# Optimization experiments

Measured on AMD Instinct MI355X. Metric: run time of the kernel, lower is better.

The kernel has to match this reference:

```python
import jax, jax.numpy as jnp
import numpy as np

T, B, I_DIM, H_DIM = 256, 64, 1024, 1024


def setup_inputs() -> dict:
    key = jax.random.key(0)
    k_in, k_wx, k_wh = jax.random.split(key, 3)
    # xavier-normal-ish scale for [hidden, input] matrices
    std_x = float(np.sqrt(2.0 / (I_DIM + H_DIM)))
    std_h = float(np.sqrt(2.0 / (H_DIM + H_DIM)))
    return {
        "inputs": jax.random.normal(k_in, (T, B, I_DIM), dtype=jnp.float32),
        "W_x": jax.random.normal(k_wx, (4, H_DIM, I_DIM), dtype=jnp.float32) * std_x,
        "W_h": jax.random.normal(k_wh, (4, H_DIM, H_DIM), dtype=jnp.float32) * std_h,
        "bias": jnp.zeros((4, H_DIM), dtype=jnp.float32),
        "mask_x": jnp.ones((4, H_DIM, I_DIM), dtype=jnp.float32),
        "mask_h": jnp.ones((4, H_DIM, H_DIM), dtype=jnp.float32),
        "H0": jnp.zeros((B, H_DIM), dtype=jnp.float32),
        "C0": jnp.zeros((B, H_DIM), dtype=jnp.float32),
    }


def reference(inputs, W_x, W_h, bias, mask_x, mask_h, H0, C0):
    # masked + transposed weights: (4, in_dim, hidden) so X @ W works
    Wx_t = jnp.transpose(W_x * mask_x, (0, 2, 1))  # (4, I, H)
    Wh_t = jnp.transpose(W_h * mask_h, (0, 2, 1))  # (4, H, H)

    # gate order per original indexing: 0=i, 1=f, 2=o, 3=c
    def step(carry, X):
        H, C = carry
        # fused gate GEMMs: (4, B, H)
        g = (jnp.einsum('bi,gih->gbh', X, Wx_t)
             + jnp.einsum('bh,ghk->gbk', H, Wh_t)
             + bias[:, None, :])
        I_g = jax.nn.sigmoid(g[0])
        F_g = jax.nn.sigmoid(g[1])
        O_g = jax.nn.sigmoid(g[2])
        C_t = jnp.tanh(g[3])
        C_new = F_g * C + I_g * C_t
        H_new = O_g * jnp.tanh(C_new)
        return (H_new, C_new), H_new

    (_, _), outputs = jax.lax.scan(step, (H0, C0), inputs)
    return outputs  # (T, B, H)
```

## Files before the change

kernel.cpp:

```cpp
#include <hip/hip_runtime.h>

typedef __attribute__((ext_vector_type(8))) short short8;
typedef __attribute__((ext_vector_type(4))) float floatx4;

#define T_STEPS 256
#define BATCH   64
#define IDIM    1024
#define HDIM    1024
#define KDIM    (IDIM + HDIM)
#define MB      16
#define HB      16
#define NWG     256
#define NTHR    512
#define A_STRIDE (KDIM + 8)

__device__ __forceinline__ unsigned short f2bf(float f) {
  unsigned u = __float_as_uint(f);
  u += 0x7FFFu + ((u >> 16) & 1u);
  return (unsigned short)(u >> 16);
}

__global__ void prep_weights(const float* __restrict__ Wx, const float* __restrict__ Wh,
                             const float* __restrict__ mx, const float* __restrict__ mh,
                             unsigned short* __restrict__ Wcat) {
  int idx = blockIdx.x * blockDim.x + threadIdx.x;
  const int total = 4 * HDIM * KDIM / 4;
  if (idx >= total) return;
  int k4 = idx & (KDIM / 4 - 1);
  int gh = idx >> 9;
  int k = k4 * 4;
  float4 v, m;
  if (k < IDIM) {
    v = *(const float4*)(Wx + (size_t)gh * IDIM + k);
    m = *(const float4*)(mx + (size_t)gh * IDIM + k);
  } else {
    v = *(const float4*)(Wh + (size_t)gh * HDIM + (k - IDIM));
    m = *(const float4*)(mh + (size_t)gh * HDIM + (k - IDIM));
  }
  ushort4 o;
  o.x = f2bf(v.x * m.x); o.y = f2bf(v.y * m.y);
  o.z = f2bf(v.z * m.z); o.w = f2bf(v.w * m.w);
  *(ushort4*)(Wcat + (size_t)gh * KDIM + k) = o;
}

__global__ void prep_h0(const float* __restrict__ H0, unsigned short* __restrict__ Hbuf0,
                        unsigned* __restrict__ cnt) {
  int i = blockIdx.x * blockDim.x + threadIdx.x;
  if (i < BATCH * HDIM) Hbuf0[i] = f2bf(H0[i]);
  if (i < 16 * 16) cnt[i] = 0u;
}

__global__ void __launch_bounds__(NTHR, 2)
lstm_main(const float* __restrict__ X,
          const float* __restrict__ bias,
          const float* __restrict__ C0,
          const unsigned short* __restrict__ Wcat,
          unsigned short* __restrict__ Hbuf0,
          unsigned short* __restrict__ Hbuf1,
          unsigned* __restrict__ cnt,
          float* __restrict__ out)
{
  __shared__ __align__(16) unsigned short Ash[MB * A_STRIDE];
  __shared__ float parts[2][4][MB][HB + 1];

  const int tid  = threadIdx.x;
  const int wg   = blockIdx.x;
  const int bg   = wg >> 6;
  const int hg   = wg & 63;
  const int b0   = bg * MB;
  const int h0   = hg * HB;

  const int w    = tid >> 6;
  const int lane = tid & 63;
  const int nl   = lane & 15;
  const int quad = lane >> 4;

  short8 Bfr[4][8];
  {
    const short8* wp = (const short8*)Wcat;
#pragma unroll
    for (int g = 0; g < 4; ++g) {
      const int rowbase = (g * HDIM + h0 + nl) * (KDIM / 8);
#pragma unroll
      for (int ks = 0; ks < 8; ++ks)
        Bfr[g][ks] = wp[rowbase + w * 32 + ks * 4 + quad];
    }
  }

  float c_state = 0.f;
  const int eb = tid >> 4;
  const int eh = tid & 15;
  if (tid < 256) c_state = C0[(b0 + eb) * HDIM + h0 + eh];

  const int e0 = tid, e1 = tid + NTHR;
  const int p0 = (e0 >> 8) * (MB * (HB + 1)) + ((e0 >> 4) & 15) * (HB + 1) + (e0 & 15);
  const int p1 = (e1 >> 8) * (MB * (HB + 1)) + ((e1 >> 4) & 15) * (HB + 1) + (e1 & 15);
  const float binit0 = bias[(e0 >> 8) * HDIM + h0 + (e0 & 15)];
  const float binit1 = bias[(e1 >> 8) * HDIM + h0 + (e1 & 15)];

  const int c8 = tid & 127;
  const int mrow = tid >> 7;

  unsigned* mycnt  = cnt + (bg * 4 + (hg & 3)) * 16;
  unsigned* bgcnt  = cnt + bg * 4 * 16;

  float4 Xpre[8];
  {
    const float4* xp = (const float4*)(X + (size_t)b0 * IDIM);
#pragma unroll
    for (int it = 0; it < 8; ++it) {
      int v = it * NTHR + tid;
      Xpre[it] = xp[(v >> 8) * (IDIM / 4) + (v & 255)];
    }
  }

  for (int t = 0; t < T_STEPS; ++t) {
    const unsigned short* __restrict__ Hprev = (t & 1) ? Hbuf1 : Hbuf0;
    unsigned short* __restrict__ Hnext       = (t & 1) ? Hbuf0 : Hbuf1;
    float* pcur = &parts[t & 1][0][0][0];

#pragma unroll
    for (int it = 0; it < 8; ++it) {
      int v = it * NTHR + tid;
      int m = v >> 8, c4 = v & 255;
      float4 f = Xpre[it];
      ushort4 o;
      o.x = f2bf(f.x); o.y = f2bf(f.y); o.z = f2bf(f.z); o.w = f2bf(f.w);
      *(ushort4*)&Ash[m * A_STRIDE + c4 * 4] = o;
    }
    pcur[p0] = binit0;
    pcur[p1] = binit1;

    if (tid == 0 && t > 0) {
      const unsigned tgt = (unsigned)(64 * t);
      for (;;) {
        unsigned s = __hip_atomic_load(bgcnt +  0, __ATOMIC_RELAXED, __HIP_MEMORY_SCOPE_AGENT)
                   + __hip_atomic_load(bgcnt + 16, __ATOMIC_RELAXED, __HIP_MEMORY_SCOPE_AGENT)
                   + __hip_atomic_load(bgcnt + 32, __ATOMIC_RELAXED, __HIP_MEMORY_SCOPE_AGENT)
                   + __hip_atomic_load(bgcnt + 48, __ATOMIC_RELAXED, __HIP_MEMORY_SCOPE_AGENT);
        if (s >= tgt) break;
        __builtin_amdgcn_s_sleep(8);
      }
    }
    __syncthreads();

    {
      const unsigned short* pa = Hprev + (size_t)(b0 + mrow) * HDIM + c8 * 8;
      uint4 d0, d1, d2, d3;
      asm volatile(
        "global_load_dwordx4 %0, %4, off sc0 sc1\n\t"
        "global_load_dwordx4 %1, %5, off sc0 sc1\n\t"
        "global_load_dwordx4 %2, %6, off sc0 sc1\n\t"
        "global_load_dwordx4 %3, %7, off sc0 sc1\n\t"
        "s_waitcnt vmcnt(0)"
        : "=&v"(d0), "=&v"(d1), "=&v"(d2), "=&v"(d3)
        : "v"(pa), "v"(pa + 4 * HDIM), "v"(pa + 8 * HDIM), "v"(pa + 12 * HDIM)
        : "memory");
      *(uint4*)&Ash[(mrow +  0) * A_STRIDE + IDIM + c8 * 8] = d0;
      *(uint4*)&Ash[(mrow +  4) * A_STRIDE + IDIM + c8 * 8] = d1;
      *(uint4*)&Ash[(mrow +  8) * A_STRIDE + IDIM + c8 * 8] = d2;
      *(uint4*)&Ash[(mrow + 12) * A_STRIDE + IDIM + c8 * 8] = d3;
    }
    __syncthreads();

    {
      int tn = (t + 1 < T_STEPS) ? t + 1 : t;
      const float4* xp = (const float4*)(X + ((size_t)tn * BATCH + b0) * IDIM);
#pragma unroll
      for (int it = 0; it < 8; ++it) {
        int v = it * NTHR + tid;
        Xpre[it] = xp[(v >> 8) * (IDIM / 4) + (v & 255)];
      }
    }

    floatx4 acc[4];
#pragma unroll
    for (int g = 0; g < 4; ++g) acc[g] = floatx4{0.f, 0.f, 0.f, 0.f};
    {
      const unsigned short* abase = &Ash[nl * A_STRIDE + w * 256 + quad * 8];
#pragma unroll
      for (int ks = 0; ks < 8; ++ks) {
        short8 af = *(const short8*)(abase + ks * 32);
#pragma unroll
        for (int g = 0; g < 4; ++g)
          acc[g] = __builtin_amdgcn_mfma_f32_16x16x32_bf16(af, Bfr[g][ks], acc[g], 0, 0, 0);
      }
    }
#pragma unroll
    for (int g = 0; g < 4; ++g)
#pragma unroll
      for (int r = 0; r < 4; ++r)
        atomicAdd(&parts[t & 1][g][quad * 4 + r][nl], acc[g][r]);
    __syncthreads();

    if (tid < 256) {
      float gI = parts[t & 1][0][eb][eh];
      float gF = parts[t & 1][1][eb][eh];
      float gO = parts[t & 1][2][eb][eh];
      float gC = parts[t & 1][3][eb][eh];
      float ig = 1.f / (1.f + __expf(-gI));
      float fg = 1.f / (1.f + __expf(-gF));
      float og = 1.f / (1.f + __expf(-gO));
      float cb = 1.f - 2.f / (__expf(2.f * gC) + 1.f);
      c_state = fg * c_state + ig * cb;
      float hn = og * (1.f - 2.f / (__expf(2.f * c_state) + 1.f));
      unsigned short hb = f2bf(hn);
      unsigned short* ps = Hnext + (size_t)(b0 + eb) * HDIM + h0 + eh;
      asm volatile("global_store_short %0, %1, off sc0 sc1"
                   :: "v"(ps), "v"((unsigned)hb) : "memory");
      out[((size_t)t * BATCH + b0 + eb) * HDIM + h0 + eh] = hn;
    }
    asm volatile("s_waitcnt vmcnt(0)" ::: "memory");
    __syncthreads();
    if (tid == 0) atomicAdd(mycnt, 1u);
  }
}

extern "C" void kernel_launch(void* const* d_in, const int* in_sizes, int n_in,
                              void* d_out, int out_size, void* d_ws, size_t ws_size,
                              hipStream_t stream) {
  const float* X    = (const float*)d_in[0];
  const float* Wx   = (const float*)d_in[1];
  const float* Wh   = (const float*)d_in[2];
  const float* bias = (const float*)d_in[3];
  const float* mx   = (const float*)d_in[4];
  const float* mh   = (const float*)d_in[5];
  const float* H0   = (const float*)d_in[6];
  const float* C0   = (const float*)d_in[7];
  float* out = (float*)d_out;

  unsigned short* Wcat  = (unsigned short*)d_ws;
  unsigned short* Hbuf0 = Wcat + (size_t)4 * HDIM * KDIM;
  unsigned short* Hbuf1 = Hbuf0 + BATCH * HDIM;
  unsigned*       cnt   = (unsigned*)(Hbuf1 + BATCH * HDIM);

  {
    int tot = 4 * HDIM * KDIM / 4;
    prep_weights<<<(tot + 255) / 256, 256, 0, stream>>>(Wx, Wh, mx, mh, Wcat);
  }
  prep_h0<<<(BATCH * HDIM + 255) / 256, 256, 0, stream>>>(H0, Hbuf0, cnt);

  void* args[] = { (void*)&X, (void*)&bias, (void*)&C0, (void*)&Wcat,
                   (void*)&Hbuf0, (void*)&Hbuf1, (void*)&cnt, (void*)&out };
  hipLaunchCooperativeKernel(reinterpret_cast<void*>(lstm_main),
                             dim3(NWG), dim3(NTHR), args, 0, stream);
}
```

Baseline: 3.477 ms.

## Split waves into X-input and H-recurrent roles, drop LDS staging and block barriers

```diff
diff --git a/kernel.cpp b/kernel.cpp
--- a/kernel.cpp
+++ b/kernel.cpp
@@ -12,7 +12,7 @@
 #define HB      16
 #define NWG     256
 #define NTHR    512
-#define A_STRIDE (KDIM + 8)
+#define NSUB    8
 
 __device__ __forceinline__ unsigned short f2bf(float f) {
   unsigned u = __float_as_uint(f);
@@ -47,7 +47,7 @@
                         unsigned* __restrict__ cnt) {
   int i = blockIdx.x * blockDim.x + threadIdx.x;
   if (i < BATCH * HDIM) Hbuf0[i] = f2bf(H0[i]);
-  if (i < 16 * 16) cnt[i] = 0u;
+  if (i < 4 * NSUB * 16) cnt[i] = 0u;
 }
 
 __global__ void __launch_bounds__(NTHR, 2)
@@ -60,7 +60,6 @@
           unsigned* __restrict__ cnt,
           float* __restrict__ out)
 {
-  __shared__ __align__(16) unsigned short Ash[MB * A_STRIDE];
   __shared__ float parts[2][4][MB][HB + 1];
 
   const int tid  = threadIdx.x;
@@ -87,105 +86,97 @@
     }
   }
 
+  for (int i = tid; i < 2 * 4 * MB * (HB + 1); i += NTHR)
+    (&parts[0][0][0][0])[i] = 0.f;
+
   float c_state = 0.f;
   const int eb = tid >> 4;
   const int eh = tid & 15;
   if (tid < 256) c_state = C0[(b0 + eb) * HDIM + h0 + eh];
 
-  const int e0 = tid, e1 = tid + NTHR;
-  const int p0 = (e0 >> 8) * (MB * (HB + 1)) + ((e0 >> 4) & 15) * (HB + 1) + (e0 & 15);
-  const int p1 = (e1 >> 8) * (MB * (HB + 1)) + ((e1 >> 4) & 15) * (HB + 1) + (e1 & 15);
-  const float binit0 = bias[(e0 >> 8) * HDIM + h0 + (e0 & 15)];
-  const float binit1 = bias[(e1 >> 8) * HDIM + h0 + (e1 & 15)];
-
-  const int c8 = tid & 127;
-  const int mrow = tid >> 7;
-
-  unsigned* mycnt  = cnt + (bg * 4 + (hg & 3)) * 16;
-  unsigned* bgcnt  = cnt + bg * 4 * 16;
-
-  float4 Xpre[8];
-  {
-    const float4* xp = (const float4*)(X + (size_t)b0 * IDIM);
-#pragma unroll
-    for (int it = 0; it < 8; ++it) {
-      int v = it * NTHR + tid;
-      Xpre[it] = xp[(v >> 8) * (IDIM / 4) + (v & 255)];
-    }
-  }
+  float sb[4];
+#pragma unroll
+  for (int g = 0; g < 4; ++g) sb[g] = bias[g * HDIM + h0 + nl];
+
+  unsigned* mycnt = cnt + (bg * NSUB + (hg & (NSUB - 1))) * 16;
+  unsigned* bgcnt = cnt + bg * NSUB * 16;
+
+  __syncthreads();
 
   for (int t = 0; t < T_STEPS; ++t) {
     const unsigned short* __restrict__ Hprev = (t & 1) ? Hbuf1 : Hbuf0;
     unsigned short* __restrict__ Hnext       = (t & 1) ? Hbuf0 : Hbuf1;
-    float* pcur = &parts[t & 1][0][0][0];
-
-#pragma unroll
-    for (int it = 0; it < 8; ++it) {
-      int v = it * NTHR + tid;
-      int m = v >> 8, c4 = v & 255;
-      float4 f = Xpre[it];
-      ushort4 o;
-      o.x = f2bf(f.x); o.y = f2bf(f.y); o.z = f2bf(f.z); o.w = f2bf(f.w);
-      *(ushort4*)&Ash[m * A_STRIDE + c4 * 4] = o;
-    }
-    pcur[p0] = binit0;
-    pcur[p1] = binit1;
-
-    if (tid == 0 && t > 0) {
-      const unsigned tgt = (unsigned)(64 * t);
-      for (;;) {
-        unsigned s = __hip_atomic_load(bgcnt +  0, __ATOMIC_RELAXED, __HIP_MEMORY_SCOPE_AGENT)
-                   + __hip_atomic_load(bgcnt + 16, __ATOMIC_RELAXED, __HIP_MEMORY_SCOPE_AGENT)
-                   + __hip_atomic_load(bgcnt + 32, __ATOMIC_RELAXED, __HIP_MEMORY_SCOPE_AGENT)
-                   + __hip_atomic_load(bgcnt + 48, __ATOMIC_RELAXED, __HIP_MEMORY_SCOPE_AGENT);
-        if (s >= tgt) break;
-        __builtin_amdgcn_s_sleep(8);
-      }
-    }
-    __syncthreads();
-
-    {
-      const unsigned short* pa = Hprev + (size_t)(b0 + mrow) * HDIM + c8 * 8;
-      uint4 d0, d1, d2, d3;
-      asm volatile(
-        "global_load_dwordx4 %0, %4, off sc0 sc1\n\t"
-        "global_load_dwordx4 %1, %5, off sc0 sc1\n\t"
-        "global_load_dwordx4 %2, %6, off sc0 sc1\n\t"
-        "global_load_dwordx4 %3, %7, off sc0 sc1\n\t"
-        "s_waitcnt vmcnt(0)"
-        : "=&v"(d0), "=&v"(d1), "=&v"(d2), "=&v"(d3)
-        : "v"(pa), "v"(pa + 4 * HDIM), "v"(pa + 8 * HDIM), "v"(pa + 12 * HDIM)
-        : "memory");
-      *(uint4*)&Ash[(mrow +  0) * A_STRIDE + IDIM + c8 * 8] = d0;
-      *(uint4*)&Ash[(mrow +  4) * A_STRIDE + IDIM + c8 * 8] = d1;
-      *(uint4*)&Ash[(mrow +  8) * A_STRIDE + IDIM + c8 * 8] = d2;
-      *(uint4*)&Ash[(mrow + 12) * A_STRIDE + IDIM + c8 * 8] = d3;
-    }
-    __syncthreads();
-
-    {
-      int tn = (t + 1 < T_STEPS) ? t + 1 : t;
-      const float4* xp = (const float4*)(X + ((size_t)tn * BATCH + b0) * IDIM);
-#pragma unroll
-      for (int it = 0; it < 8; ++it) {
-        int v = it * NTHR + tid;
-        Xpre[it] = xp[(v >> 8) * (IDIM / 4) + (v & 255)];
-      }
-    }
 
     floatx4 acc[4];
 #pragma unroll
     for (int g = 0; g < 4; ++g) acc[g] = floatx4{0.f, 0.f, 0.f, 0.f};
-    {
-      const unsigned short* abase = &Ash[nl * A_STRIDE + w * 256 + quad * 8];
+
+    if (w < 4) {
+      const uint4* u = (const uint4*)(X + ((size_t)t * BATCH + b0 + nl) * IDIM
+                                        + w * 256 + quad * 8);
 #pragma unroll
       for (int ks = 0; ks < 8; ++ks) {
-        short8 af = *(const short8*)(abase + ks * 32);
+        uint4 lo = u[ks * 8];
+        uint4 hi = u[ks * 8 + 1];
+        short8 af;
+        af[0] = (short)f2bf(__uint_as_float(lo.x));
+        af[1] = (short)f2bf(__uint_as_float(lo.y));
+        af[2] = (short)f2bf(__uint_as_float(lo.z));
+        af[3] = (short)f2bf(__uint_as_float(lo.w));
+        af[4] = (short)f2bf(__uint_as_float(hi.x));
+        af[5] = (short)f2bf(__uint_as_float(hi.y));
+        af[6] = (short)f2bf(__uint_as_float(hi.z));
+        af[7] = (short)f2bf(__uint_as_float(hi.w));
 #pragma unroll
         for (int g = 0; g < 4; ++g)
           acc[g] = __builtin_amdgcn_mfma_f32_16x16x32_bf16(af, Bfr[g][ks], acc[g], 0, 0, 0);
       }
-    }
+      if (w == 0) {
+#pragma unroll
+        for (int g = 0; g < 4; ++g)
+#pragma unroll
+          for (int r = 0; r < 4; ++r)
+            acc[g][r] += sb[g];
+      }
+    } else {
+      if (t > 0) {
+        const unsigned tgt = 256u * (unsigned)t;
+        for (;;) {
+          unsigned s = 0;
+#pragma unroll
+          for (int k = 0; k < NSUB; ++k)
+            s += __hip_atomic_load(bgcnt + k * 16, __ATOMIC_RELAXED, __HIP_MEMORY_SCOPE_AGENT);
+          if (s >= tgt) break;
+          __builtin_amdgcn_s_sleep(2);
+        }
+      }
+      const unsigned short* hb = Hprev + (size_t)(b0 + nl) * HDIM + (w - 4) * 256 + quad * 8;
+      uint4 hq0, hq1, hq2, hq3, hq4, hq5, hq6, hq7;
+      asm volatile(
+        "global_load_dwordx4 %0, %8, off sc0 sc1\n\t"
+        "global_load_dwordx4 %1, %8, off offset:64 sc0 sc1\n\t"
+        "global_load_dwordx4 %2, %8, off offset:128 sc0 sc1\n\t"
+        "global_load_dwordx4 %3, %8, off offset:192 sc0 sc1\n\t"
+        "global_load_dwordx4 %4, %8, off offset:256 sc0 sc1\n\t"
+        "global_load_dwordx4 %5, %8, off offset:320 sc0 sc1\n\t"
+        "global_load_dwordx4 %6, %8, off offset:384 sc0 sc1\n\t"
+        "global_load_dwordx4 %7, %8, off offset:448 sc0 sc1\n\t"
+        "s_waitcnt vmcnt(0)"
+        : "=&v"(hq0), "=&v"(hq1), "=&v"(hq2), "=&v"(hq3),
+          "=&v"(hq4), "=&v"(hq5), "=&v"(hq6), "=&v"(hq7)
+        : "v"(hb)
+        : "memory");
+      union { uint4 u; short8 s; } cv;
+      uint4 hq[8] = { hq0, hq1, hq2, hq3, hq4, hq5, hq6, hq7 };
+#pragma unroll
+      for (int ks = 0; ks < 8; ++ks) {
+        cv.u = hq[ks];
+#pragma unroll
+        for (int g = 0; g < 4; ++g)
+          acc[g] = __builtin_amdgcn_mfma_f32_16x16x32_bf16(cv.s, Bfr[g][ks], acc[g], 0, 0, 0);
+      }
+    }
+
 #pragma unroll
     for (int g = 0; g < 4; ++g)
 #pragma unroll
@@ -194,10 +185,10 @@
     __syncthreads();
 
     if (tid < 256) {
-      float gI = parts[t & 1][0][eb][eh];
-      float gF = parts[t & 1][1][eb][eh];
-      float gO = parts[t & 1][2][eb][eh];
-      float gC = parts[t & 1][3][eb][eh];
+      float gI = parts[t & 1][0][eb][eh]; parts[t & 1][0][eb][eh] = 0.f;
+      float gF = parts[t & 1][1][eb][eh]; parts[t & 1][1][eb][eh] = 0.f;
+      float gO = parts[t & 1][2][eb][eh]; parts[t & 1][2][eb][eh] = 0.f;
+      float gC = parts[t & 1][3][eb][eh]; parts[t & 1][3][eb][eh] = 0.f;
       float ig = 1.f / (1.f + __expf(-gI));
       float fg = 1.f / (1.f + __expf(-gF));
       float og = 1.f / (1.f + __expf(-gO));
@@ -210,9 +201,11 @@
                    :: "v"(ps), "v"((unsigned)hb) : "memory");
       out[((size_t)t * BATCH + b0 + eb) * HDIM + h0 + eh] = hn;
     }
-    asm volatile("s_waitcnt vmcnt(0)" ::: "memory");
-    __syncthreads();
-    if (tid == 0) atomicAdd(mycnt, 1u);
+    if (w < 4) {
+      asm volatile("s_waitcnt vmcnt(0)" ::: "memory");
+      if (lane == 0)
+        __hip_atomic_fetch_add(mycnt, 1u, __ATOMIC_RELAXED, __HIP_MEMORY_SCOPE_AGENT);
+    }
   }
 }
 
```

Result: slower. 4.503 ms (+29.5%).
